# Optimization experiments

Hardware: AMD Instinct MI355X
Metric: run time of the kernel (lower is better)

The kernel has to match this reference:

```python
import jax, jax.numpy as jnp
import numpy as np
import math

B, T, C = 2, 2048, 2048
H, G, HS = 16, 4, 128  # n_head, n_query_groups, head_size
EPS = 1e-5
SCALE = 1.0 / math.sqrt(HS)
QKV_DIM = (H + 2 * G) * HS  # 3072, gate logits (H) appended after


def _build_rope(seq_len, n_elem, base):
    freq = base ** (np.arange(0, n_elem, 2, dtype=np.float64) / n_elem)
    inv_freq = 1.0 / freq
    idx_theta = np.outer(np.arange(seq_len, dtype=np.float64), inv_freq)
    return (jnp.asarray(np.cos(idx_theta), dtype=jnp.float32),
            jnp.asarray(np.sin(idx_theta), dtype=jnp.float32))


def setup_inputs() -> dict:
    key = jax.random.key(0)
    k1, k2, k3 = jax.random.split(key, 3)
    x = jax.random.normal(k1, (B, T, C), dtype=jnp.float32)
    # rope base per module: 0.09 * local_window ** 1.628
    base = 0.09 * (2048.0 ** 1.628)
    cos, sin = _build_rope(T, HS, base)  # [T, HS//2]
    W_attn = jax.random.normal(k2, (QKV_DIM + H, C), dtype=jnp.float32) * 0.02
    W_proj = jax.random.normal(k3, (C, H * HS), dtype=jnp.float32) * 0.02
    q_norm_w = jnp.ones((HS,), dtype=jnp.float32)
    k_norm_w = jnp.ones((HS,), dtype=jnp.float32)
    return {"x": x, "cos": cos, "sin": sin, "W_attn": W_attn,
            "q_norm_w": q_norm_w, "k_norm_w": k_norm_w, "W_proj": W_proj}


def _rms_norm(v, w):
    # per-head RMSNorm over last dim (head_size)
    ms = jnp.mean(jnp.square(v), axis=-1, keepdims=True)
    return v * jax.lax.rsqrt(ms + EPS) * w


def _apply_rope(v, cos, sin):
    # v: [B, T, N, HS]; cos/sin: [T, HS//2]; non-interleaved halves
    d2 = v.shape[-1] // 2
    x1, x2 = v[..., :d2], v[..., d2:]
    c = cos[None, :, None, :]
    s = sin[None, :, None, :]
    return jnp.concatenate([x1 * c - x2 * s, x2 * c + x1 * s], axis=-1)


def reference(x, cos, sin, W_attn, q_norm_w, k_norm_w, W_proj):
    qkv = jnp.einsum('btc,oc->bto', x, W_attn)  # [B, T, QKV_DIM+H]
    q = qkv[..., : H * HS].reshape(B, T, H, HS)
    k = qkv[..., H * HS:(H + G) * HS].reshape(B, T, G, HS)
    v = qkv[..., (H + G) * HS: QKV_DIM].reshape(B, T, G, HS)
    gate = qkv[..., QKV_DIM:]  # [B, T, H]

    q = _apply_rope(_rms_norm(q, q_norm_w), cos, sin)
    k = _apply_rope(_rms_norm(k, k_norm_w), cos, sin)

    rep = H // G
    kr = jnp.repeat(k, rep, axis=2)  # [B, T, H, HS]
    vr = jnp.repeat(v, rep, axis=2)

    scores = jnp.einsum('bthd,bshd->bhts', q, kr) * SCALE  # [B, H, T, T]
    causal = jnp.tril(jnp.ones((T, T), dtype=bool))
    scores = jnp.where(causal, scores, jnp.finfo(scores.dtype).min)
    probs = jax.nn.softmax(scores, axis=-1)
    out = jnp.einsum('bhts,bshd->bthd', probs, vr)  # [B, T, H, HS]

    out = out * jax.nn.sigmoid(gate)[..., None]  # gated attention, per-head
    y = jnp.einsum('bto,co->btc', out.reshape(B, T, H * HS), W_proj)
    return y
```

## Files before the change

kernel.cpp:

```cpp
#include <hip/hip_runtime.h>

#define T_   2048
#define BB   2
#define CC   2048
#define HH   16
#define GG   4
#define HSS  128
#define QKVD 3072
#define NQKV 3088
#define NPAD 3200
#define SCALE_ 0.08838834764831845f
#define SCALE2_ (0.08838834764831845f * 1.4426950408889634f)

typedef __attribute__((ext_vector_type(8))) short  short8;
typedef __attribute__((ext_vector_type(4))) float  f32x4;
typedef __attribute__((ext_vector_type(4))) int    v4i;
typedef __attribute__((ext_vector_type(4))) float  v4f;
typedef __attribute__((ext_vector_type(4))) unsigned short u16x4;

typedef const void __attribute__((address_space(1)))* gas1_t;
typedef void __attribute__((address_space(3)))* as3_t;

__device__ __forceinline__ void gl_lds16(const void* g, void* l) {
    __builtin_amdgcn_global_load_lds((gas1_t)g, (as3_t)l, 16, 0, 0);
}

__device__ __forceinline__ unsigned short f2bf(float f) {
    unsigned u = __float_as_uint(f);
    u += 0x7fffu + ((u >> 16) & 1u);
    return (unsigned short)(u >> 16);
}
__device__ __forceinline__ float bf2f(unsigned short h) {
    return __uint_as_float(((unsigned)h) << 16);
}

template <int CTRL>
__device__ __forceinline__ float dppmv(float x) {
    int i = __float_as_int(x);
    return __int_as_float(__builtin_amdgcn_update_dpp(i, i, CTRL, 0xF, 0xF, false));
}
__device__ __forceinline__ void red16_max(float* v) {
#pragma unroll
    for (int r = 0; r < 4; ++r) v[r] = fmaxf(v[r], dppmv<0xB1>(v[r]));
#pragma unroll
    for (int r = 0; r < 4; ++r) v[r] = fmaxf(v[r], dppmv<0x4E>(v[r]));
#pragma unroll
    for (int r = 0; r < 4; ++r) v[r] = fmaxf(v[r], dppmv<0x124>(v[r]));
#pragma unroll
    for (int r = 0; r < 4; ++r) v[r] = fmaxf(v[r], dppmv<0x128>(v[r]));
}
__device__ __forceinline__ void red16_sum(float* v) {
#pragma unroll
    for (int r = 0; r < 4; ++r) v[r] += dppmv<0xB1>(v[r]);
#pragma unroll
    for (int r = 0; r < 4; ++r) v[r] += dppmv<0x4E>(v[r]);
#pragma unroll
    for (int r = 0; r < 4; ++r) v[r] += dppmv<0x124>(v[r]);
#pragma unroll
    for (int r = 0; r < 4; ++r) v[r] += dppmv<0x128>(v[r]);
}

__global__ void k_convert(const float* __restrict__ src, unsigned short* __restrict__ dst,
                          int n_src4, int n_dst4) {
    int i = blockIdx.x * blockDim.x + threadIdx.x;
    if (i >= n_dst4) return;
    u16x4 o;
    if (i < n_src4) {
        v4f v = *(const v4f*)(src + (size_t)i * 4);
        o[0] = f2bf(v[0]); o[1] = f2bf(v[1]); o[2] = f2bf(v[2]); o[3] = f2bf(v[3]);
    } else {
        o[0] = 0; o[1] = 0; o[2] = 0; o[3] = 0;
    }
    *(u16x4*)(dst + (size_t)i * 4) = o;
}

template <int BM_, typename OutT>
__launch_bounds__(512, 2)
__global__ void k_gemm8(const unsigned short* __restrict__ A,
                        const unsigned short* __restrict__ Bm,
                        OutT* __restrict__ C,
                        int K, int lda, int ldb, int ldc, int nmax) {
    constexpr int MI  = BM_ / 32;
    constexpr int NPH = MI / 2;
    __shared__ unsigned short As[2][BM_ * 64];
    __shared__ unsigned short Bs[2][256 * 64];
    const int t = threadIdx.x;
    const int lane = t & 63;
    const int wid  = t >> 6;
    const int wr = wid >> 2, wc = wid & 3;
    const int bm = blockIdx.x, bn = blockIdx.y;
    const int fro = lane & 15, fk = lane >> 4;

    const int srow  = lane >> 3;
    const size_t scol = (size_t)(((lane & 7) ^ srow) * 8);

    const unsigned short* Abase = A  + (size_t)(bm * BM_) * lda;
    const unsigned short* Bbase = Bm + (size_t)(bn * 256) * ldb;

    f32x4 acc[MI][4];
#pragma unroll
    for (int i = 0; i < MI; ++i)
#pragma unroll
        for (int j = 0; j < 4; ++j) acc[i][j] = (f32x4){0.f, 0.f, 0.f, 0.f};

#pragma unroll
    for (int h = 0; h < 2; ++h)
#pragma unroll
        for (int c8 = 0; c8 < 2; ++c8) {
            const int rr = h * 128 + wid * 16 + c8 * 8;
            if (BM_ == 256 || h == 0)
                gl_lds16(Abase + (size_t)(rr + srow) * lda + scol, &As[0][rr * 64]);
            gl_lds16(Bbase + (size_t)(rr + srow) * ldb + scol, &Bs[0][rr * 64]);
        }

    int cur = 0;
    for (int kt = 0; kt < K; kt += 64) {
        asm volatile("s_waitcnt vmcnt(0)" ::: "memory");
        __builtin_amdgcn_s_barrier();
        __builtin_amdgcn_sched_barrier(0);
        const bool pf = (kt + 64 < K);
        const int nxt = cur ^ 1;
        const int kn = kt + 64;

        short8 bf_[4][2];
#pragma unroll
        for (int q = 0; q < NPH; ++q) {
            short8 af[2][2];
#pragma unroll
            for (int im = 0; im < 2; ++im)
#pragma unroll
                for (int kk = 0; kk < 2; ++kk) {
                    const int ar = wr * (BM_ / 2) + (q * 2 + im) * 16 + fro;
                    af[im][kk] = *(const short8*)&As[cur][ar * 64 + ((kk * 4 + fk) ^ (ar & 7)) * 8];
                }
            if (q == 0) {
#pragma unroll
                for (int ni = 0; ni < 4; ++ni)
#pragma unroll
                    for (int kk = 0; kk < 2; ++kk) {
                        const int br = wc * 64 + ni * 16 + fro;
                        bf_[ni][kk] = *(const short8*)&Bs[cur][br * 64 + ((kk * 4 + fk) ^ (br & 7)) * 8];
                    }
            }
            if (pf) {
                if (BM_ == 256) {
                    const int h = q & 1;
#pragma unroll
                    for (int c8 = 0; c8 < 2; ++c8) {
                        const int rr = h * 128 + wid * 16 + c8 * 8;
                        if ((q >> 1) == 0)
                            gl_lds16(Abase + (size_t)(rr + srow) * lda + kn + scol, &As[nxt][rr * 64]);
                        else
                            gl_lds16(Bbase + (size_t)(rr + srow) * ldb + kn + scol, &Bs[nxt][rr * 64]);
                    }
                } else {
                    if (q == 0) {
#pragma unroll
                        for (int c8 = 0; c8 < 2; ++c8) {
                            const int rr = wid * 16 + c8 * 8;
                            gl_lds16(Abase + (size_t)(rr + srow) * lda + kn + scol, &As[nxt][rr * 64]);
                        }
                    } else {
#pragma unroll
                        for (int h = 0; h < 2; ++h)
#pragma unroll
                            for (int c8 = 0; c8 < 2; ++c8) {
                                const int rr = h * 128 + wid * 16 + c8 * 8;
                                gl_lds16(Bbase + (size_t)(rr + srow) * ldb + kn + scol, &Bs[nxt][rr * 64]);
                            }
                    }
                }
            }
            __builtin_amdgcn_s_setprio(1);
#pragma unroll
            for (int im = 0; im < 2; ++im)
#pragma unroll
                for (int ni = 0; ni < 4; ++ni)
#pragma unroll
                    for (int kk = 0; kk < 2; ++kk)
                        acc[q * 2 + im][ni] = __builtin_amdgcn_mfma_f32_16x16x32_bf16(
                            af[im][kk], bf_[ni][kk], acc[q * 2 + im][ni], 0, 0, 0);
            __builtin_amdgcn_s_setprio(0);
            __builtin_amdgcn_s_barrier();
        }
        cur ^= 1;
    }

    const int col16 = lane & 15, rbase = (lane >> 4) * 4;
    const int gr0 = bm * BM_ + wr * (BM_ / 2);
    const int gc0 = bn * 256 + wc * 64;
#pragma unroll
    for (int mi = 0; mi < MI; ++mi)
#pragma unroll
        for (int ni = 0; ni < 4; ++ni) {
            const int gcol = gc0 + ni * 16 + col16;
            if (gcol < nmax) {
#pragma unroll
                for (int r = 0; r < 4; ++r) {
                    const int grow = gr0 + mi * 16 + rbase + r;
                    float v = acc[mi][ni][r];
                    if constexpr (sizeof(OutT) == 2)
                        C[(size_t)grow * ldc + gcol] = (OutT)f2bf(v);
                    else
                        C[(size_t)grow * ldc + gcol] = (OutT)v;
                }
            }
        }
}

__global__ void k_normrope(unsigned short* __restrict__ qkv,
                           const float* __restrict__ cosT, const float* __restrict__ sinT,
                           const float* __restrict__ qw, const float* __restrict__ kw) {
    const int lane = threadIdx.x & 63;
    const int row  = blockIdx.x * 4 + (threadIdx.x >> 6);
    const int tok  = row / 20;
    const int hh   = row - tok * 20;
    const int tpos = tok & (T_ - 1);
    unsigned short* rp = qkv + (size_t)tok * NPAD + (hh < 16 ? hh * 128 : 2048 + (hh - 16) * 128);
    const float* w = (hh < 16) ? qw : kw;
    float e1 = bf2f(rp[lane]);
    float e2 = bf2f(rp[lane + 64]);
    float ss = e1 * e1 + e2 * e2;
#pragma unroll
    for (int m = 1; m < 64; m <<= 1) ss += __shfl_xor(ss, m);
    float inv = rsqrtf(ss * (1.0f / 128.0f) + 1e-5f);
    float n1 = e1 * inv * w[lane];
    float n2 = e2 * inv * w[lane + 64];
    float c = cosT[tpos * 64 + lane];
    float s = sinT[tpos * 64 + lane];
    rp[lane]      = f2bf(n1 * c - n2 * s);
    rp[lane + 64] = f2bf(n2 * c + n1 * s);
}

__global__ void k_transposeV(const unsigned short* __restrict__ qkv,
                             unsigned short* __restrict__ vt) {
    __shared__ unsigned short tile[64][65];
    const int b = blockIdx.x >> 2, g = blockIdx.x & 3;
    const int s0 = blockIdx.y * 64, d0 = blockIdx.z * 64;
    const int tx = threadIdx.x & 63, ty0 = threadIdx.x >> 6;
    const unsigned short* src = qkv + (size_t)(b * T_ + s0) * NPAD + 2560 + g * 128 + d0;
#pragma unroll
    for (int r = 0; r < 16; ++r) {
        int ty = ty0 * 16 + r;
        tile[ty][tx] = src[(size_t)ty * NPAD + tx];
    }
    __syncthreads();
    unsigned short* dstp = vt + ((size_t)(b * GG + g) * 128 + d0) * T_ + s0;
#pragma unroll
    for (int r = 0; r < 16; ++r) {
        int ty = ty0 * 16 + r;
        dstp[(size_t)ty * T_ + tx] = tile[tx][ty];
    }
}

__launch_bounds__(256, 2)
__global__ void k_attn(const unsigned short* __restrict__ qkv,
                       const unsigned short* __restrict__ vt,
                       unsigned short* __restrict__ ao) {
    __shared__ unsigned short Ks[2][64 * 128];
    __shared__ unsigned short Vs[2][128 * 64];
    __shared__ unsigned short Ps[4][16 * 72];
    const int t = threadIdx.x;
    const int lane = t & 63;
    const int wid  = t >> 6;
    const int id = blockIdx.x;
    const int bg = id & 7;
    const int hh = (id >> 3) & 3;
    const int pr = id >> 5;
    const int b = bg >> 2, g = bg & 3, h = g * 4 + hh;
    const int fro = lane & 15, fk = lane >> 4;
    const int rbase = fk * 4;

    const unsigned short* kg0 = qkv + (size_t)(b * T_) * NPAD + 2048 + g * 128;
    const unsigned short* vg0 = vt + (size_t)(b * GG + g) * 128 * T_;

    const int cp0 = wid * 4;
    int cur = 0;

#pragma unroll
    for (int seg = 0; seg < 2; ++seg) {
        const int qt = (seg == 0) ? pr : 31 - pr;
        const int q0w = qt * 64 + wid * 16;

        short8 qf[4];
        const unsigned short* qp = qkv + (size_t)(b * T_ + q0w + fro) * NPAD + h * 128 + fk * 8;
#pragma unroll
        for (int kb = 0; kb < 4; ++kb) qf[kb] = *(const short8*)(qp + kb * 32);

        float m_r[4], l_r[4];
        f32x4 o[8];
#pragma unroll
        for (int r = 0; r < 4; ++r) { m_r[r] = -1e30f; l_r[r] = 0.f; }
#pragma unroll
        for (int d = 0; d < 8; ++d) o[d] = (f32x4){0.f, 0.f, 0.f, 0.f};

        const int nt = qt + 1;

#pragma unroll
        for (int p = 0; p < 4; ++p) {
            const int cp = cp0 + p;
            const int kr = cp * 4 + (lane >> 4);
            const int sK = lane & 15;
            gl_lds16(kg0 + (size_t)kr * NPAD + (size_t)((sK ^ (kr & 7)) * 8), &Ks[cur][cp * 512]);
            const int d  = cp * 8 + (lane >> 3);
            const int sV = lane & 7;
            gl_lds16(vg0 + (size_t)d * T_ + (size_t)((sV ^ (d & 7)) * 8), &Vs[cur][cp * 512]);
        }
        __syncthreads();

        for (int ti = 0; ti < nt; ++ti) {
            if (ti + 1 < nt) {
                const int sn = (ti + 1) * 64;
#pragma unroll
                for (int p = 0; p < 4; ++p) {
                    const int cp = cp0 + p;
                    const int kr = cp * 4 + (lane >> 4);
                    const int sK = lane & 15;
                    gl_lds16(kg0 + (size_t)(sn + kr) * NPAD + (size_t)((sK ^ (kr & 7)) * 8), &Ks[cur ^ 1][cp * 512]);
                    const int d  = cp * 8 + (lane >> 3);
                    const int sV = lane & 7;
                    gl_lds16(vg0 + (size_t)d * T_ + sn + (size_t)((sV ^ (d & 7)) * 8), &Vs[cur ^ 1][cp * 512]);
                }
            }
            f32x4 sc[4];
#pragma unroll
            for (int jb = 0; jb < 4; ++jb) sc[jb] = (f32x4){0.f, 0.f, 0.f, 0.f};
#pragma unroll
            for (int jb = 0; jb < 4; ++jb) {
                const int kr = jb * 16 + fro;
#pragma unroll
                for (int kb = 0; kb < 4; ++kb) {
                    short8 kf = *(const short8*)&Ks[cur][kr * 128 + 8 * ((kb * 4 + fk) ^ (kr & 7))];
                    sc[jb] = __builtin_amdgcn_mfma_f32_16x16x32_bf16(qf[kb], kf, sc[jb], 0, 0, 0);
                }
            }
            const bool domask = (ti == qt);
#pragma unroll
            for (int jb = 0; jb < 4; ++jb)
#pragma unroll
                for (int r = 0; r < 4; ++r) {
                    float v = sc[jb][r] * SCALE2_;
                    if (domask && (jb * 16 + fro) > (wid * 16 + rbase + r)) v = -1e30f;
                    sc[jb][r] = v;
                }
            float mx[4], fs[4], rs[4];
#pragma unroll
            for (int r = 0; r < 4; ++r)
                mx[r] = fmaxf(fmaxf(sc[0][r], sc[1][r]), fmaxf(sc[2][r], sc[3][r]));
            red16_max(mx);
#pragma unroll
            for (int r = 0; r < 4; ++r) {
                float mn = fmaxf(m_r[r], mx[r]);
                fs[r] = exp2f(m_r[r] - mn);
                m_r[r] = mn;
            }
#pragma unroll
            for (int jb = 0; jb < 4; ++jb)
#pragma unroll
                for (int r = 0; r < 4; ++r) sc[jb][r] = exp2f(sc[jb][r] - m_r[r]);
#pragma unroll
            for (int r = 0; r < 4; ++r)
                rs[r] = (sc[0][r] + sc[1][r]) + (sc[2][r] + sc[3][r]);
            red16_sum(rs);
#pragma unroll
            for (int r = 0; r < 4; ++r) l_r[r] = l_r[r] * fs[r] + rs[r];
#pragma unroll
            for (int d = 0; d < 8; ++d)
#pragma unroll
                for (int r = 0; r < 4; ++r) o[d][r] *= fs[r];
            unsigned short* pw = &Ps[wid][0];
#pragma unroll
            for (int jb = 0; jb < 4; ++jb)
#pragma unroll
                for (int r = 0; r < 4; ++r)
                    pw[(rbase + r) * 72 + jb * 16 + fro] = f2bf(sc[jb][r]);
            asm volatile("s_waitcnt lgkmcnt(0)" ::: "memory");
            __builtin_amdgcn_sched_barrier(0);
            short8 pa[2];
#pragma unroll
            for (int ks = 0; ks < 2; ++ks)
                pa[ks] = *(const short8*)&Ps[wid][fro * 72 + ks * 32 + fk * 8];
#pragma unroll
            for (int ks = 0; ks < 2; ++ks)
#pragma unroll
                for (int db = 0; db < 8; ++db) {
                    const int d = db * 16 + fro;
                    short8 vf = *(const short8*)&Vs[cur][d * 64 + 8 * ((ks * 4 + fk) ^ (d & 7))];
                    o[db] = __builtin_amdgcn_mfma_f32_16x16x32_bf16(pa[ks], vf, o[db], 0, 0, 0);
                }
            __syncthreads();
            cur ^= 1;
        }
#pragma unroll
        for (int r = 0; r < 4; ++r) {
            const int qrow = q0w + rbase + r;
            float gv = bf2f(qkv[(size_t)(b * T_ + qrow) * NPAD + QKVD + h]);
            float sg = 1.f / (1.f + __expf(-gv));
            float invl = sg / l_r[r];
            unsigned short* orow = ao + (size_t)(b * T_ + qrow) * 2048 + h * 128;
#pragma unroll
            for (int db = 0; db < 8; ++db)
                orow[db * 16 + fro] = f2bf(o[db][r] * invl);
        }
    }
}

extern "C" void kernel_launch(void* const* d_in, const int* in_sizes, int n_in,
                              void* d_out, int out_size, void* d_ws, size_t ws_size,
                              hipStream_t stream) {
    const float* x      = (const float*)d_in[0];
    const float* cosT   = (const float*)d_in[1];
    const float* sinT   = (const float*)d_in[2];
    const float* W_attn = (const float*)d_in[3];
    const float* qw     = (const float*)d_in[4];
    const float* kw     = (const float*)d_in[5];
    const float* W_proj = (const float*)d_in[6];

    char* ws = (char*)d_ws;
    const size_t OFF_XB   = 0;
    const size_t OFF_WAB  = 16777216;
    const size_t OFF_WPB  = 29884416;
    const size_t OFF_QKV  = 38273024;
    const size_t OFF_VT   = 64487424;
    const size_t OFF_AO   = 68681728;
    const size_t NEED     = 85458944;
    if (ws_size < NEED) return;

    unsigned short* xb   = (unsigned short*)(ws + OFF_XB);
    unsigned short* wab  = (unsigned short*)(ws + OFF_WAB);
    unsigned short* wpb  = (unsigned short*)(ws + OFF_WPB);
    unsigned short* qkvb = (unsigned short*)(ws + OFF_QKV);
    unsigned short* vtb  = (unsigned short*)(ws + OFF_VT);
    unsigned short* aob  = (unsigned short*)(ws + OFF_AO);

    k_convert<<<8192, 256, 0, stream>>>(x,      xb,  2097152, 2097152);
    k_convert<<<6400, 256, 0, stream>>>(W_attn, wab, 1581056, 1638400);
    k_convert<<<4096, 256, 0, stream>>>(W_proj, wpb, 1048576, 1048576);
    k_gemm8<256, unsigned short><<<dim3(16, 13), 512, 0, stream>>>(xb, wab, qkvb, 2048, 2048, 2048, NPAD, NPAD);
    k_normrope<<<20480, 256, 0, stream>>>(qkvb, cosT, sinT, qw, kw);
    k_transposeV<<<dim3(8, 32, 2), 256, 0, stream>>>(qkvb, vtb);
    k_attn<<<512, 256, 0, stream>>>(qkvb, vtb, aob);
    k_gemm8<128, float><<<dim3(32, 8), 512, 0, stream>>>(aob, wpb, (float*)d_out, 2048, 2048, 2048, 2048, 2048);
}
```

Measured before the change: 224.4 us.

## Single-buffer attention tiles and launch one block per query tile for occupancy

The attention kernel drops the double-buffered K/V LDS prefetch and the paired-segment scheme, where each block handled two query tiles to balance causal work. It now launches 1024 blocks, one per 64-row query tile, ordered longest-first. It raises launch bounds to 4 blocks per CU and swizzles the P scratch buffer to avoid LDS bank conflicts. The aim is to hide latency through occupancy rather than software prefetch, at the cost of exposed load latency within each block and an extra barrier per iteration.

```diff
diff --git a/kernel.cpp b/kernel.cpp
--- a/kernel.cpp
+++ b/kernel.cpp
@@ -253,155 +253,139 @@
     }
 }
 
-__launch_bounds__(256, 2)
+__launch_bounds__(256, 4)
 __global__ void k_attn(const unsigned short* __restrict__ qkv,
                        const unsigned short* __restrict__ vt,
                        unsigned short* __restrict__ ao) {
-    __shared__ unsigned short Ks[2][64 * 128];
-    __shared__ unsigned short Vs[2][128 * 64];
-    __shared__ unsigned short Ps[4][16 * 72];
+    __shared__ unsigned short Ks[64 * 128];
+    __shared__ unsigned short Vs[128 * 64];
+    __shared__ unsigned short Ps[4][16 * 64];
     const int t = threadIdx.x;
     const int lane = t & 63;
     const int wid  = t >> 6;
     const int id = blockIdx.x;
     const int bg = id & 7;
     const int hh = (id >> 3) & 3;
-    const int pr = id >> 5;
+    const int qi = id >> 5;
+    const int qt = 31 - qi;
     const int b = bg >> 2, g = bg & 3, h = g * 4 + hh;
     const int fro = lane & 15, fk = lane >> 4;
     const int rbase = fk * 4;
+    const int q0w = qt * 64 + wid * 16;
 
     const unsigned short* kg0 = qkv + (size_t)(b * T_) * NPAD + 2048 + g * 128;
     const unsigned short* vg0 = vt + (size_t)(b * GG + g) * 128 * T_;
 
+    short8 qf[4];
+    const unsigned short* qp = qkv + (size_t)(b * T_ + q0w + fro) * NPAD + h * 128 + fk * 8;
+#pragma unroll
+    for (int kb = 0; kb < 4; ++kb) qf[kb] = *(const short8*)(qp + kb * 32);
+
+    float m_r[4], l_r[4];
+    f32x4 o[8];
+#pragma unroll
+    for (int r = 0; r < 4; ++r) { m_r[r] = -1e30f; l_r[r] = 0.f; }
+#pragma unroll
+    for (int d = 0; d < 8; ++d) o[d] = (f32x4){0.f, 0.f, 0.f, 0.f};
+
+    const int nt = qt + 1;
     const int cp0 = wid * 4;
-    int cur = 0;
-
-#pragma unroll
-    for (int seg = 0; seg < 2; ++seg) {
-        const int qt = (seg == 0) ? pr : 31 - pr;
-        const int q0w = qt * 64 + wid * 16;
-
-        short8 qf[4];
-        const unsigned short* qp = qkv + (size_t)(b * T_ + q0w + fro) * NPAD + h * 128 + fk * 8;
-#pragma unroll
-        for (int kb = 0; kb < 4; ++kb) qf[kb] = *(const short8*)(qp + kb * 32);
-
-        float m_r[4], l_r[4];
-        f32x4 o[8];
-#pragma unroll
-        for (int r = 0; r < 4; ++r) { m_r[r] = -1e30f; l_r[r] = 0.f; }
-#pragma unroll
-        for (int d = 0; d < 8; ++d) o[d] = (f32x4){0.f, 0.f, 0.f, 0.f};
-
-        const int nt = qt + 1;
-
+
+    for (int ti = 0; ti < nt; ++ti) {
+        const int s0 = ti * 64;
+        __syncthreads();
 #pragma unroll
         for (int p = 0; p < 4; ++p) {
             const int cp = cp0 + p;
             const int kr = cp * 4 + (lane >> 4);
             const int sK = lane & 15;
-            gl_lds16(kg0 + (size_t)kr * NPAD + (size_t)((sK ^ (kr & 7)) * 8), &Ks[cur][cp * 512]);
+            gl_lds16(kg0 + (size_t)(s0 + kr) * NPAD + (size_t)((sK ^ (kr & 7)) * 8), &Ks[cp * 512]);
             const int d  = cp * 8 + (lane >> 3);
             const int sV = lane & 7;
-            gl_lds16(vg0 + (size_t)d * T_ + (size_t)((sV ^ (d & 7)) * 8), &Vs[cur][cp * 512]);
+            gl_lds16(vg0 + (size_t)d * T_ + s0 + (size_t)((sV ^ (d & 7)) * 8), &Vs[cp * 512]);
         }
         __syncthreads();
 
-        for (int ti = 0; ti < nt; ++ti) {
-            if (ti + 1 < nt) {
-                const int sn = (ti + 1) * 64;
-#pragma unroll
-                for (int p = 0; p < 4; ++p) {
-                    const int cp = cp0 + p;
-                    const int kr = cp * 4 + (lane >> 4);
-                    const int sK = lane & 15;
-                    gl_lds16(kg0 + (size_t)(sn + kr) * NPAD + (size_t)((sK ^ (kr & 7)) * 8), &Ks[cur ^ 1][cp * 512]);
-                    const int d  = cp * 8 + (lane >> 3);
-                    const int sV = lane & 7;
-                    gl_lds16(vg0 + (size_t)d * T_ + sn + (size_t)((sV ^ (d & 7)) * 8), &Vs[cur ^ 1][cp * 512]);
-                }
-            }
-            f32x4 sc[4];
-#pragma unroll
-            for (int jb = 0; jb < 4; ++jb) sc[jb] = (f32x4){0.f, 0.f, 0.f, 0.f};
-#pragma unroll
-            for (int jb = 0; jb < 4; ++jb) {
-                const int kr = jb * 16 + fro;
-#pragma unroll
-                for (int kb = 0; kb < 4; ++kb) {
-                    short8 kf = *(const short8*)&Ks[cur][kr * 128 + 8 * ((kb * 4 + fk) ^ (kr & 7))];
-                    sc[jb] = __builtin_amdgcn_mfma_f32_16x16x32_bf16(qf[kb], kf, sc[jb], 0, 0, 0);
-                }
-            }
-            const bool domask = (ti == qt);
-#pragma unroll
-            for (int jb = 0; jb < 4; ++jb)
-#pragma unroll
-                for (int r = 0; r < 4; ++r) {
-                    float v = sc[jb][r] * SCALE2_;
-                    if (domask && (jb * 16 + fro) > (wid * 16 + rbase + r)) v = -1e30f;
-                    sc[jb][r] = v;
-                }
-            float mx[4], fs[4], rs[4];
-#pragma unroll
-            for (int r = 0; r < 4; ++r)
-                mx[r] = fmaxf(fmaxf(sc[0][r], sc[1][r]), fmaxf(sc[2][r], sc[3][r]));
-            red16_max(mx);
+        f32x4 sc[4];
+#pragma unroll
+        for (int jb = 0; jb < 4; ++jb) sc[jb] = (f32x4){0.f, 0.f, 0.f, 0.f};
+#pragma unroll
+        for (int jb = 0; jb < 4; ++jb) {
+            const int kr = jb * 16 + fro;
+#pragma unroll
+            for (int kb = 0; kb < 4; ++kb) {
+                short8 kf = *(const short8*)&Ks[kr * 128 + 8 * ((kb * 4 + fk) ^ (kr & 7))];
+                sc[jb] = __builtin_amdgcn_mfma_f32_16x16x32_bf16(qf[kb], kf, sc[jb], 0, 0, 0);
+            }
+        }
+        const bool domask = (ti == qt);
+#pragma unroll
+        for (int jb = 0; jb < 4; ++jb)
 #pragma unroll
             for (int r = 0; r < 4; ++r) {
-                float mn = fmaxf(m_r[r], mx[r]);
-                fs[r] = exp2f(m_r[r] - mn);
-                m_r[r] = mn;
-            }
-#pragma unroll
-            for (int jb = 0; jb < 4; ++jb)
-#pragma unroll
-                for (int r = 0; r < 4; ++r) sc[jb][r] = exp2f(sc[jb][r] - m_r[r]);
-#pragma unroll
-            for (int r = 0; r < 4; ++r)
-                rs[r] = (sc[0][r] + sc[1][r]) + (sc[2][r] + sc[3][r]);
-            red16_sum(rs);
-#pragma unroll
-            for (int r = 0; r < 4; ++r) l_r[r] = l_r[r] * fs[r] + rs[r];
-#pragma unroll
-            for (int d = 0; d < 8; ++d)
-#pragma unroll
-                for (int r = 0; r < 4; ++r) o[d][r] *= fs[r];
-            unsigned short* pw = &Ps[wid][0];
-#pragma unroll
-            for (int jb = 0; jb < 4; ++jb)
-#pragma unroll
-                for (int r = 0; r < 4; ++r)
-                    pw[(rbase + r) * 72 + jb * 16 + fro] = f2bf(sc[jb][r]);
-            asm volatile("s_waitcnt lgkmcnt(0)" ::: "memory");
-            __builtin_amdgcn_sched_barrier(0);
-            short8 pa[2];
-#pragma unroll
-            for (int ks = 0; ks < 2; ++ks)
-                pa[ks] = *(const short8*)&Ps[wid][fro * 72 + ks * 32 + fk * 8];
-#pragma unroll
-            for (int ks = 0; ks < 2; ++ks)
-#pragma unroll
-                for (int db = 0; db < 8; ++db) {
-                    const int d = db * 16 + fro;
-                    short8 vf = *(const short8*)&Vs[cur][d * 64 + 8 * ((ks * 4 + fk) ^ (d & 7))];
-                    o[db] = __builtin_amdgcn_mfma_f32_16x16x32_bf16(pa[ks], vf, o[db], 0, 0, 0);
-                }
-            __syncthreads();
-            cur ^= 1;
-        }
+                float v = sc[jb][r] * SCALE2_;
+                if (domask && (jb * 16 + fro) > (wid * 16 + rbase + r)) v = -1e30f;
+                sc[jb][r] = v;
+            }
+        float mx[4], fs[4], rs[4];
+#pragma unroll
+        for (int r = 0; r < 4; ++r)
+            mx[r] = fmaxf(fmaxf(sc[0][r], sc[1][r]), fmaxf(sc[2][r], sc[3][r]));
+        red16_max(mx);
 #pragma unroll
         for (int r = 0; r < 4; ++r) {
-            const int qrow = q0w + rbase + r;
-            float gv = bf2f(qkv[(size_t)(b * T_ + qrow) * NPAD + QKVD + h]);
-            float sg = 1.f / (1.f + __expf(-gv));
-            float invl = sg / l_r[r];
-            unsigned short* orow = ao + (size_t)(b * T_ + qrow) * 2048 + h * 128;
-#pragma unroll
-            for (int db = 0; db < 8; ++db)
-                orow[db * 16 + fro] = f2bf(o[db][r] * invl);
-        }
+            float mn = fmaxf(m_r[r], mx[r]);
+            fs[r] = exp2f(m_r[r] - mn);
+            m_r[r] = mn;
+        }
+#pragma unroll
+        for (int jb = 0; jb < 4; ++jb)
+#pragma unroll
+            for (int r = 0; r < 4; ++r) sc[jb][r] = exp2f(sc[jb][r] - m_r[r]);
+#pragma unroll
+        for (int r = 0; r < 4; ++r)
+            rs[r] = (sc[0][r] + sc[1][r]) + (sc[2][r] + sc[3][r]);
+        red16_sum(rs);
+#pragma unroll
+        for (int r = 0; r < 4; ++r) l_r[r] = l_r[r] * fs[r] + rs[r];
+#pragma unroll
+        for (int d = 0; d < 8; ++d)
+#pragma unroll
+            for (int r = 0; r < 4; ++r) o[d][r] *= fs[r];
+        unsigned short* pw = &Ps[wid][0];
+#pragma unroll
+        for (int jb = 0; jb < 4; ++jb)
+#pragma unroll
+            for (int r = 0; r < 4; ++r) {
+                const int row = rbase + r;
+                const int slot = jb * 2 + (fro >> 3);
+                pw[row * 64 + ((slot ^ (row & 7)) * 8 + (fro & 7))] = f2bf(sc[jb][r]);
+            }
+        asm volatile("s_waitcnt lgkmcnt(0)" ::: "memory");
+        __builtin_amdgcn_sched_barrier(0);
+        short8 pa[2];
+#pragma unroll
+        for (int ks = 0; ks < 2; ++ks)
+            pa[ks] = *(const short8*)&Ps[wid][fro * 64 + ((ks * 4 + fk) ^ (fro & 7)) * 8];
+#pragma unroll
+        for (int ks = 0; ks < 2; ++ks)
+#pragma unroll
+            for (int db = 0; db < 8; ++db) {
+                const int d = db * 16 + fro;
+                short8 vf = *(const short8*)&Vs[d * 64 + 8 * ((ks * 4 + fk) ^ (d & 7))];
+                o[db] = __builtin_amdgcn_mfma_f32_16x16x32_bf16(pa[ks], vf, o[db], 0, 0, 0);
+            }
+    }
+#pragma unroll
+    for (int r = 0; r < 4; ++r) {
+        const int qrow = q0w + rbase + r;
+        float gv = bf2f(qkv[(size_t)(b * T_ + qrow) * NPAD + QKVD + h]);
+        float sg = 1.f / (1.f + __expf(-gv));
+        float invl = sg / l_r[r];
+        unsigned short* orow = ao + (size_t)(b * T_ + qrow) * 2048 + h * 128;
+#pragma unroll
+        for (int db = 0; db < 8; ++db)
+            orow[db * 16 + fro] = f2bf(o[db][r] * invl);
     }
 }
 
@@ -439,6 +423,6 @@
     k_gemm8<256, unsigned short><<<dim3(16, 13), 512, 0, stream>>>(xb, wab, qkvb, 2048, 2048, 2048, NPAD, NPAD);
     k_normrope<<<20480, 256, 0, stream>>>(qkvb, cosT, sinT, qw, kw);
     k_transposeV<<<dim3(8, 32, 2), 256, 0, stream>>>(qkvb, vtb);
-    k_attn<<<512, 256, 0, stream>>>(qkvb, vtb, aob);
+    k_attn<<<1024, 256, 0, stream>>>(qkvb, vtb, aob);
     k_gemm8<128, float><<<dim3(32, 8), 512, 0, stream>>>(aob, wpb, (float*)d_out, 2048, 2048, 2048, 2048, 2048);
 }
```

New measurement: 233.4 us. 4.0% more time.
